# Optimization experiments

Hardware: AMD Instinct MI355X
Metric: run time of the kernel (lower is better)

Reference implementation:

```python
import jax, jax.numpy as jnp
import numpy as np

B, C, H, W = 8, 320, 32, 32
HEADS, DHEAD = 8, 40
CTX_LEN, CTX_DIM = 77, 768
FF_INNER = 4 * C
GROUPS = 32
HW = H * W


def setup_inputs() -> dict:
    key = jax.random.key(0)
    ks = jax.random.split(key, 16)
    def nrm(k, shape, s=0.02):
        return (jax.random.normal(k, shape) * s).astype(jnp.float32)
    z = lambda *s: jnp.zeros(s, jnp.float32)
    o = lambda *s: jnp.ones(s, jnp.float32)
    inp = {}
    inp["x"] = jax.random.normal(ks[0], (B, C, H, W), jnp.float32)
    inp["context"] = jax.random.normal(ks[1], (B, CTX_LEN, CTX_DIM), jnp.float32)
    inp["vis_mask"] = jax.random.uniform(ks[2], (B, HW, HW)) > 0.5
    inp["v2t_mask"] = jax.random.uniform(ks[3], (B, HW, CTX_LEN)) > 0.5
    inp["gn_scale"] = o(C); inp["gn_bias"] = z(C)
    inp["proj_in_w"] = nrm(ks[4], (C, C)); inp["proj_in_b"] = z(C)
    inp["n1_s"] = o(C); inp["n1_b"] = z(C)
    inp["wq1"] = nrm(ks[5], (C, C)); inp["wk1"] = nrm(ks[6], (C, C)); inp["wv1"] = nrm(ks[7], (C, C))
    inp["wo1"] = nrm(ks[8], (C, C)); inp["bo1"] = z(C)
    inp["n2_s"] = o(C); inp["n2_b"] = z(C)
    inp["wq2"] = nrm(ks[9], (C, C)); inp["wk2"] = nrm(ks[10], (CTX_DIM, C)); inp["wv2"] = nrm(ks[11], (CTX_DIM, C))
    inp["wo2"] = nrm(ks[12], (C, C)); inp["bo2"] = z(C)
    inp["n3_s"] = o(C); inp["n3_b"] = z(C)
    inp["ff_w1"] = nrm(ks[13], (C, 2 * FF_INNER)); inp["ff_b1"] = z(2 * FF_INNER)
    inp["ff_w2"] = nrm(ks[14], (FF_INNER, C)); inp["ff_b2"] = z(C)
    inp["proj_out_w"] = nrm(ks[15], (C, C)); inp["proj_out_b"] = z(C)
    return inp


def group_norm(x, scale, bias, eps=1e-6):
    b, c, h, w = x.shape
    xg = x.reshape(b, GROUPS, -1)
    mu = xg.mean(-1, keepdims=True)
    var = xg.var(-1, keepdims=True)
    xn = ((xg - mu) * jax.lax.rsqrt(var + eps)).reshape(b, c, h, w)
    return xn * scale[None, :, None, None] + bias[None, :, None, None]


def layer_norm(x, s, b, eps=1e-5):
    mu = x.mean(-1, keepdims=True)
    var = x.var(-1, keepdims=True)
    return (x - mu) * jax.lax.rsqrt(var + eps) * s + b


def mha(xq, ctx, wq, wk, wv, wo, bo, mask):
    # CrossAttention: manual einsum softmax with boolean mask broadcast over heads
    b, n, _ = xq.shape
    m = ctx.shape[1]
    split = lambda t: t.reshape(b, -1, HEADS, DHEAD).transpose(0, 2, 1, 3)
    q = split(xq @ wq)   # [b,h,n,d]
    k = split(ctx @ wk)  # [b,h,m,d]
    v = split(ctx @ wv)
    sim = jnp.einsum('bhid,bhjd->bhij', q, k) * (DHEAD ** -0.5)
    if mask is not None:
        sim = jnp.where(mask[:, None, :, :], sim, jnp.finfo(sim.dtype).min)
    attn = jax.nn.softmax(sim, axis=-1)
    out = jnp.einsum('bhij,bhjd->bhid', attn, v)
    out = out.transpose(0, 2, 1, 3).reshape(b, n, HEADS * DHEAD)
    return out @ wo + bo


def reference(x, context, vis_mask, v2t_mask, gn_scale, gn_bias, proj_in_w, proj_in_b,
              n1_s, n1_b, wq1, wk1, wv1, wo1, bo1,
              n2_s, n2_b, wq2, wk2, wv2, wo2, bo2,
              n3_s, n3_b, ff_w1, ff_b1, ff_w2, ff_b2,
              proj_out_w, proj_out_b):
    x_in = x
    h = group_norm(x, gn_scale, gn_bias)
    # 1x1 conv proj_in == per-pixel linear; flatten b c h w -> b (hw) c
    h = h.reshape(B, C, HW).transpose(0, 2, 1) @ proj_in_w + proj_in_b
    # masked self-attention (vis mask)
    h = h + mha(layer_norm(h, n1_s, n1_b), layer_norm(h, n1_s, n1_b),
                wq1, wk1, wv1, wo1, bo1, vis_mask)
    # masked cross-attention to text (v2t mask)
    h = h + mha(layer_norm(h, n2_s, n2_b), context,
                wq2, wk2, wv2, wo2, bo2, v2t_mask)
    # GEGLU feedforward (glu=True, mult=4)
    y = layer_norm(h, n3_s, n3_b) @ ff_w1 + ff_b1
    a, g = jnp.split(y, 2, axis=-1)
    h = h + (a * jax.nn.gelu(g, approximate=False)) @ ff_w2 + ff_b2
    # proj_out + residual
    out = (h @ proj_out_w + proj_out_b).transpose(0, 2, 1).reshape(B, C, H, W)
    return out + x_in
```

## Files before the change

### kernel.cpp

```cpp
#include <hip/hip_runtime.h>
#include <hip/hip_bf16.h>
#include <math.h>


#define Bsz   8
#define Cch   320
#define HW    1024
#define NTOK  (Bsz*HW)
#define HEADS 8
#define DHEAD 40
#define CTXL  77
#define CTXD  768
#define FFI   1280
#define MCTX  (Bsz*CTXL)
#define MCTXP 640

typedef unsigned short u16;
typedef unsigned long long u64;
typedef __attribute__((ext_vector_type(8))) u16    u16x8;
typedef __attribute__((ext_vector_type(8))) __bf16 bf16x8;
typedef __attribute__((ext_vector_type(4))) float  f32x4;

__device__ inline u16 f2b(float f) {
    unsigned u = __float_as_uint(f);
    return (u16)((u + 0x7FFFu + ((u >> 16) & 1u)) >> 16);
}

__global__ __launch_bounds__(256) void gn_apply(
    const float* __restrict__ x, const float* __restrict__ gnA,
    const float* __restrict__ gnB, u16* __restrict__ out)
{
    __shared__ u16 T[64*72];
    const int tid = threadIdx.x;
    const int c0 = blockIdx.x * 64;
    const int p0 = blockIdx.y * 64;
    const int b  = blockIdx.z;
    for (int e = tid; e < 512; e += 256) {
        int r = e >> 3, ch = e & 7;
        const float* src = x + ((size_t)(b*Cch + c0 + r))*HW + p0 + ch*8;
        float a  = gnA[b*Cch + c0 + r];
        float bb = gnB[b*Cch + c0 + r];
        float4 v0 = *(const float4*)src;
        float4 v1 = *(const float4*)(src + 4);
        u16x8 val;
        val[0] = f2b(v0.x*a + bb); val[1] = f2b(v0.y*a + bb);
        val[2] = f2b(v0.z*a + bb); val[3] = f2b(v0.w*a + bb);
        val[4] = f2b(v1.x*a + bb); val[5] = f2b(v1.y*a + bb);
        val[6] = f2b(v1.z*a + bb); val[7] = f2b(v1.w*a + bb);
        *(u16x8*)&T[r*72 + (ch ^ (r & 7))*8] = val;
    }
    __syncthreads();
    for (int e = tid; e < 4096; e += 256) {
        int p = e >> 6, c = e & 63;
        u16 v = T[c*72 + (((p >> 3) ^ (c & 7))*8) + (p & 7)];
        out[((size_t)(b*HW + p0 + p))*Cch + c0 + c] = v;
    }
}

__global__ __launch_bounds__(256) void layernorm_kernel(
    const float* __restrict__ in, const float* __restrict__ s,
    const float* __restrict__ bgain, u16* __restrict__ out)
{
    int t = blockIdx.x*4 + (threadIdx.x >> 6);
    int lane = threadIdx.x & 63;
    const float* row = in + (size_t)t*Cch;
    float v[5];
    float sum = 0.f, sq = 0.f;
    #pragma unroll
    for (int i = 0; i < 5; ++i) {
        v[i] = row[lane + 64*i];
        sum += v[i]; sq += v[i]*v[i];
    }
    #pragma unroll
    for (int off = 32; off > 0; off >>= 1) {
        sum += __shfl_xor(sum, off);
        sq  += __shfl_xor(sq,  off);
    }
    float mean = sum * (1.f/320.f);
    float var  = sq  * (1.f/320.f) - mean*mean;
    float inv  = rsqrtf(var + 1e-5f);
    u16* orow = out + (size_t)t*Cch;
    #pragma unroll
    for (int i = 0; i < 5; ++i) {
        int c = lane + 64*i;
        orow[c] = f2b((v[i]-mean)*inv*s[c] + bgain[c]);
    }
}

struct WDesc { const float* src; u16* dst; int K; int N; int tiles; float scl; };
struct WPack { WDesc w[12]; };

#define WT_TILES 620
#define CTXBLK   240

__global__ __launch_bounds__(256) void preamble(
    WPack p, const float* __restrict__ ctxsrc, u16* __restrict__ ctxdst,
    const void* __restrict__ vis, const void* __restrict__ v2t,
    u64* __restrict__ bvis, u64* __restrict__ bv2t,
    const float* __restrict__ x, const float* __restrict__ gscale,
    const float* __restrict__ gbias, float* __restrict__ gnA,
    float* __restrict__ gnB)
{
    __shared__ u16 T[64*72];
    int blk = blockIdx.x;
    int tid = threadIdx.x;
    if (blk < WT_TILES) {
        int t = blk;
        #pragma unroll
        for (int i = 0; i < 12; ++i) {
            int nt = p.w[i].tiles;
            if (t < nt) {
                const int K = p.w[i].K, N = p.w[i].N;
                const int ntN = N >> 6;
                const int tk = t / ntN, tn = t - tk*ntN;
                const float scl = p.w[i].scl;
                const float* src = p.w[i].src;
                u16* dst = p.w[i].dst;
                for (int e = tid; e < 512; e += 256) {
                    int r = e >> 3, ch = e & 7;
                    const float* sp = src + (size_t)(tk*64 + r)*N + tn*64 + ch*8;
                    float4 v0 = *(const float4*)sp;
                    float4 v1 = *(const float4*)(sp + 4);
                    u16x8 val;
                    val[0] = f2b(v0.x*scl); val[1] = f2b(v0.y*scl);
                    val[2] = f2b(v0.z*scl); val[3] = f2b(v0.w*scl);
                    val[4] = f2b(v1.x*scl); val[5] = f2b(v1.y*scl);
                    val[6] = f2b(v1.z*scl); val[7] = f2b(v1.w*scl);
                    *(u16x8*)&T[r*72 + (ch ^ (r & 7))*8] = val;
                }
                __syncthreads();
                for (int e = tid; e < 4096; e += 256) {
                    int n = e >> 6, k = e & 63;
                    u16 v = T[k*72 + (((n >> 3) ^ (k & 7))*8) + (n & 7)];
                    dst[(size_t)(tn*64 + n)*K + tk*64 + k] = v;
                }
                return;
            }
            t -= nt;
        }
        return;
    }
    if (blk < WT_TILES + CTXBLK) {
        int idx = (blk - WT_TILES)*2048 + tid*8;
        int r = idx / CTXD;
        u16x8 val = {};
        if (r < MCTX) {
            float4 v0 = *(const float4*)(ctxsrc + idx);
            float4 v1 = *(const float4*)(ctxsrc + idx + 4);
            val[0] = f2b(v0.x); val[1] = f2b(v0.y);
            val[2] = f2b(v0.z); val[3] = f2b(v0.w);
            val[4] = f2b(v1.x); val[5] = f2b(v1.y);
            val[6] = f2b(v1.z); val[7] = f2b(v1.w);
        }
        *(u16x8*)(ctxdst + idx) = val;
        return;
    }
    if (blk >= WT_TILES + CTXBLK + 4096) {
        int gb = blk - (WT_TILES + CTXBLK + 4096);
        int b = gb >> 5, g = gb & 31;
        __shared__ float rs[256], rq[256];
        const float4* xg = (const float4*)(x + ((size_t)b*Cch + g*10)*HW);
        float s = 0.f, q = 0.f;
        #pragma unroll
        for (int i = 0; i < 10; ++i) {
            float4 v = xg[tid + i*256];
            s += v.x + v.y + v.z + v.w;
            q += v.x*v.x + v.y*v.y + v.z*v.z + v.w*v.w;
        }
        rs[tid] = s; rq[tid] = q; __syncthreads();
        for (int off = 128; off > 0; off >>= 1) {
            if (tid < off) { rs[tid] += rs[tid+off]; rq[tid] += rq[tid+off]; }
            __syncthreads();
        }
        if (tid < 10) {
            float mean = rs[0] * (1.f/10240.f);
            float var  = rq[0] * (1.f/10240.f) - mean*mean;
            float inv  = rsqrtf(var + 1e-6f);
            int chn = g*10 + tid;
            float a = inv * gscale[chn];
            gnA[b*Cch + chn] = a;
            gnB[b*Cch + chn] = gbias[chn] - mean*a;
        }
        return;
    }
    __shared__ int any;
    if (tid == 0) any = 0;
    __syncthreads();
    const unsigned char* probe = (const unsigned char*)vis;
    for (int i = tid; i < 4096; i += 256)
        if ((i & 3) && probe[i]) any = 1;
    __syncthreads();
    const int isU8 = any;
    int mb = blk - WT_TILES - CTXBLK;
    const void* mask; u64* bits; int Lkv, nw;
    if (mb < 2048) { mask = vis; bits = bvis; Lkv = HW;   nw = 16; }
    else           { mask = v2t; bits = bv2t; Lkv = CTXL; nw = 2; mb -= 2048; }
    const int wv = tid >> 6, lane = tid & 63;
    const int row = mb*4 + wv;
    const unsigned char* m8  = (const unsigned char*)mask;
    const int*           m32 = (const int*)mask;
    const size_t base = (size_t)row * Lkv;
    for (int w = 0; w < nw; ++w) {
        int j = w*64 + lane;
        bool on = (j < Lkv) && (isU8 ? (m8[base+j] != 0) : (m32[base+j] != 0));
        u64 word = __ballot(on);
        if (lane == 0) bits[(size_t)row*nw + w] = word;
    }
}

__global__ __launch_bounds__(512) void gemm_bf16(
    const u16* __restrict__ A, const u16* __restrict__ Wt,
    const float* __restrict__ bias, const float* __restrict__ res,
    float* __restrict__ out, u16* __restrict__ out_bf, int M, int N, int K)
{
    __shared__ u16 As[2][128*40];
    __shared__ u16 Bs[2][64*40];
    const int tid  = threadIdx.x;
    const int lane = tid & 63;
    const int w    = tid >> 6;
    const int mp   = w >> 1;
    const int np   = w & 1;
    const int m0   = blockIdx.x * 128;
    const int n0   = blockIdx.y * 64;
    const int fr   = lane & 15, fg = lane >> 4;
    const int ar   = tid >> 2, ac = tid & 3;
    const bool hasB = tid < 256;

    const u16* pa = A  + (size_t)(m0 + ar)*K + ac*8;
    const u16* pb = Wt + (size_t)(n0 + ar)*K + ac*8;
    const int nk = K >> 5;

    *(u16x8*)&As[0][ar*40 + ac*8] = *(const u16x8*)pa;
    if (hasB) *(u16x8*)&Bs[0][ar*40 + ac*8] = *(const u16x8*)pb;
    u16x8 xa = *(const u16x8*)(pa + 32);
    u16x8 ya = *(const u16x8*)(pa + 64);
    u16x8 xb = {}, yb = {};
    if (hasB) { xb = *(const u16x8*)(pb + 32); yb = *(const u16x8*)(pb + 64); }

    f32x4 acc[2][2] = {};
    for (int i = 0; i < nk; i += 2) {
        __syncthreads();
        *(u16x8*)&As[1][ar*40 + ac*8] = xa;
        if (hasB) *(u16x8*)&Bs[1][ar*40 + ac*8] = xb;
        if (i + 3 < nk) {
            xa = *(const u16x8*)(pa + 32*(i+3));
            if (hasB) xb = *(const u16x8*)(pb + 32*(i+3));
        }
        {
            bf16x8 a0 = *(const bf16x8*)&As[0][(mp*32      + fr)*40 + fg*8];
            bf16x8 a1 = *(const bf16x8*)&As[0][(mp*32 + 16 + fr)*40 + fg*8];
            #pragma unroll
            for (int t = 0; t < 2; ++t) {
                bf16x8 b = *(const bf16x8*)&Bs[0][((np*2+t)*16 + fr)*40 + fg*8];
                acc[0][t] = __builtin_amdgcn_mfma_f32_16x16x32_bf16(a0, b, acc[0][t], 0, 0, 0);
                acc[1][t] = __builtin_amdgcn_mfma_f32_16x16x32_bf16(a1, b, acc[1][t], 0, 0, 0);
            }
        }
        __syncthreads();
        if (i + 2 < nk) {
            *(u16x8*)&As[0][ar*40 + ac*8] = ya;
            if (hasB) *(u16x8*)&Bs[0][ar*40 + ac*8] = yb;
            if (i + 4 < nk) {
                ya = *(const u16x8*)(pa + 32*(i+4));
                if (hasB) yb = *(const u16x8*)(pb + 32*(i+4));
            }
        }
        {
            bf16x8 a0 = *(const bf16x8*)&As[1][(mp*32      + fr)*40 + fg*8];
            bf16x8 a1 = *(const bf16x8*)&As[1][(mp*32 + 16 + fr)*40 + fg*8];
            #pragma unroll
            for (int t = 0; t < 2; ++t) {
                bf16x8 b = *(const bf16x8*)&Bs[1][((np*2+t)*16 + fr)*40 + fg*8];
                acc[0][t] = __builtin_amdgcn_mfma_f32_16x16x32_bf16(a0, b, acc[0][t], 0, 0, 0);
                acc[1][t] = __builtin_amdgcn_mfma_f32_16x16x32_bf16(a1, b, acc[1][t], 0, 0, 0);
            }
        }
    }
    #pragma unroll
    for (int at = 0; at < 2; ++at) {
        #pragma unroll
        for (int t = 0; t < 2; ++t) {
            int gn = n0 + (np*2+t)*16 + fr;
            float bv = bias ? bias[gn] : 0.f;
            #pragma unroll
            for (int i = 0; i < 4; ++i) {
                int gm = m0 + mp*32 + at*16 + fg*4 + i;
                float v = acc[at][t][i] + bv;
                if (res) v += res[(size_t)gm*N + gn];
                if (out) out[(size_t)gm*N + gn] = v;
                if (out_bf) out_bf[(size_t)gm*N + gn] = f2b(v);
            }
        }
    }
}

__global__ __launch_bounds__(512) void gemm_qkv_ctx(
    const u16* __restrict__ A, const u16* __restrict__ Wt,
    u16* __restrict__ out_bf,
    const u16* __restrict__ ctx, const u16* __restrict__ wk,
    const u16* __restrict__ wv, u16* __restrict__ kout, u16* __restrict__ vout)
{
    __shared__ u16 As[2][128*40];
    __shared__ u16 Bs[2][64*40];
    const int tid  = threadIdx.x;
    const int lane = tid & 63;
    const int w    = tid >> 6;
    const int fr   = lane & 15, fg = lane >> 4;
    const int bi   = blockIdx.x;

    if (bi < 960) {
        const int K  = Cch, N = 960;
        const int m0 = (bi & 63)*128;
        const int n0 = (bi >> 6)*64;
        const int mp = w >> 1, np = w & 1;
        const int ar = tid >> 2, ac = tid & 3;
        const bool hasB = tid < 256;

        const u16* pa = A  + (size_t)(m0 + ar)*K + ac*8;
        const u16* pb = Wt + (size_t)(n0 + ar)*K + ac*8;
        const int nk = K >> 5;

        *(u16x8*)&As[0][ar*40 + ac*8] = *(const u16x8*)pa;
        if (hasB) *(u16x8*)&Bs[0][ar*40 + ac*8] = *(const u16x8*)pb;
        u16x8 xa = *(const u16x8*)(pa + 32);
        u16x8 ya = *(const u16x8*)(pa + 64);
        u16x8 xb = {}, yb = {};
        if (hasB) { xb = *(const u16x8*)(pb + 32); yb = *(const u16x8*)(pb + 64); }

        f32x4 acc[2][2] = {};
        for (int i = 0; i < nk; i += 2) {
            __syncthreads();
            *(u16x8*)&As[1][ar*40 + ac*8] = xa;
            if (hasB) *(u16x8*)&Bs[1][ar*40 + ac*8] = xb;
            if (i + 3 < nk) {
                xa = *(const u16x8*)(pa + 32*(i+3));
                if (hasB) xb = *(const u16x8*)(pb + 32*(i+3));
            }
            {
                bf16x8 a0 = *(const bf16x8*)&As[0][(mp*32      + fr)*40 + fg*8];
                bf16x8 a1 = *(const bf16x8*)&As[0][(mp*32 + 16 + fr)*40 + fg*8];
                #pragma unroll
                for (int t = 0; t < 2; ++t) {
                    bf16x8 b = *(const bf16x8*)&Bs[0][((np*2+t)*16 + fr)*40 + fg*8];
                    acc[0][t] = __builtin_amdgcn_mfma_f32_16x16x32_bf16(a0, b, acc[0][t], 0, 0, 0);
                    acc[1][t] = __builtin_amdgcn_mfma_f32_16x16x32_bf16(a1, b, acc[1][t], 0, 0, 0);
                }
            }
            __syncthreads();
            if (i + 2 < nk) {
                *(u16x8*)&As[0][ar*40 + ac*8] = ya;
                if (hasB) *(u16x8*)&Bs[0][ar*40 + ac*8] = yb;
                if (i + 4 < nk) {
                    ya = *(const u16x8*)(pa + 32*(i+4));
                    if (hasB) yb = *(const u16x8*)(pb + 32*(i+4));
                }
            }
            {
                bf16x8 a0 = *(const bf16x8*)&As[1][(mp*32      + fr)*40 + fg*8];
                bf16x8 a1 = *(const bf16x8*)&As[1][(mp*32 + 16 + fr)*40 + fg*8];
                #pragma unroll
                for (int t = 0; t < 2; ++t) {
                    bf16x8 b = *(const bf16x8*)&Bs[1][((np*2+t)*16 + fr)*40 + fg*8];
                    acc[0][t] = __builtin_amdgcn_mfma_f32_16x16x32_bf16(a0, b, acc[0][t], 0, 0, 0);
                    acc[1][t] = __builtin_amdgcn_mfma_f32_16x16x32_bf16(a1, b, acc[1][t], 0, 0, 0);
                }
            }
        }
        #pragma unroll
        for (int at = 0; at < 2; ++at) {
            #pragma unroll
            for (int t = 0; t < 2; ++t) {
                int gn = n0 + (np*2+t)*16 + fr;
                #pragma unroll
                for (int i = 0; i < 4; ++i) {
                    int gm = m0 + mp*32 + at*16 + fg*4 + i;
                    out_bf[(size_t)gm*N + gn] = f2b(acc[at][t][i]);
                }
            }
        }
        return;
    }

    {
        int cb = bi - 960;
        const int z  = cb / 50; cb -= z*50;
        const int my = cb / 5, nx0 = cb - my*5;
        const int m0 = my*64, n0 = nx0*64;
        const u16* Wt2 = z ? wv : wk;
        u16* outp      = z ? vout : kout;
        const int mg = w >> 1;
        const int np = w & 1;
        const bool isA = tid < 256;
        const int cr = (tid & 255) >> 2, cc = tid & 3;

        const u16* ps = isA ? ctx + (size_t)(m0 + cr)*CTXD + cc*8
                            : Wt2 + (size_t)(n0 + cr)*CTXD + cc*8;
        u16* s0 = isA ? &As[0][cr*40 + cc*8] : &Bs[0][cr*40 + cc*8];
        u16* s1 = isA ? &As[1][cr*40 + cc*8] : &Bs[1][cr*40 + cc*8];
        const int nk = CTXD >> 5;

        *(u16x8*)s0 = *(const u16x8*)ps;
        u16x8 xv = *(const u16x8*)(ps + 32);
        u16x8 yv = *(const u16x8*)(ps + 64);

        f32x4 acc[2] = {};
        for (int i = 0; i < nk; i += 2) {
            __syncthreads();
            *(u16x8*)s1 = xv;
            if (i + 3 < nk) xv = *(const u16x8*)(ps + 32*(i+3));
            {
                bf16x8 a = *(const bf16x8*)&As[0][(mg*16 + fr)*40 + fg*8];
                #pragma unroll
                for (int t = 0; t < 2; ++t) {
                    bf16x8 b = *(const bf16x8*)&Bs[0][((np*2+t)*16 + fr)*40 + fg*8];
                    acc[t] = __builtin_amdgcn_mfma_f32_16x16x32_bf16(a, b, acc[t], 0, 0, 0);
                }
            }
            __syncthreads();
            if (i + 2 < nk) {
                *(u16x8*)s0 = yv;
                if (i + 4 < nk) yv = *(const u16x8*)(ps + 32*(i+4));
            }
            {
                bf16x8 a = *(const bf16x8*)&As[1][(mg*16 + fr)*40 + fg*8];
                #pragma unroll
                for (int t = 0; t < 2; ++t) {
                    bf16x8 b = *(const bf16x8*)&Bs[1][((np*2+t)*16 + fr)*40 + fg*8];
                    acc[t] = __builtin_amdgcn_mfma_f32_16x16x32_bf16(a, b, acc[t], 0, 0, 0);
                }
            }
        }
        #pragma unroll
        for (int t = 0; t < 2; ++t) {
            int gn = n0 + (np*2+t)*16 + fr;
            #pragma unroll
            for (int i = 0; i < 4; ++i) {
                int gm = m0 + mg*16 + fg*4 + i;
                if (gm < MCTX)
                    outp[(size_t)gm*Cch + gn] = f2b(acc[t][i]);
            }
        }
    }
}

__global__ __launch_bounds__(512) void gemm_pout(
    const u16* __restrict__ A, const u16* __restrict__ Wt,
    const float* __restrict__ bias, const float* __restrict__ x,
    float* __restrict__ out, int K)
{
    __shared__ u16 As[2][128*40];
    __shared__ u16 Bs[2][64*40];
    const int tid  = threadIdx.x;
    const int lane = tid & 63;
    const int w    = tid >> 6;
    const int mp   = w >> 1;
    const int np   = w & 1;
    const int m0   = blockIdx.x * 128;
    const int n0   = blockIdx.y * 64;
    const int fr   = lane & 15, fg = lane >> 4;
    const int ar   = tid >> 2, ac = tid & 3;
    const bool hasB = tid < 256;

    const u16* pa = A  + (size_t)(m0 + ar)*K + ac*8;
    const u16* pb = Wt + (size_t)(n0 + ar)*K + ac*8;
    const int nk = K >> 5;

    *(u16x8*)&As[0][ar*40 + ac*8] = *(const u16x8*)pa;
    if (hasB) *(u16x8*)&Bs[0][ar*40 + ac*8] = *(const u16x8*)pb;
    u16x8 xa = *(const u16x8*)(pa + 32);
    u16x8 ya = *(const u16x8*)(pa + 64);
    u16x8 xb = {}, yb = {};
    if (hasB) { xb = *(const u16x8*)(pb + 32); yb = *(const u16x8*)(pb + 64); }

    f32x4 acc[2][2] = {};
    for (int i = 0; i < nk; i += 2) {
        __syncthreads();
        *(u16x8*)&As[1][ar*40 + ac*8] = xa;
        if (hasB) *(u16x8*)&Bs[1][ar*40 + ac*8] = xb;
        if (i + 3 < nk) {
            xa = *(const u16x8*)(pa + 32*(i+3));
            if (hasB) xb = *(const u16x8*)(pb + 32*(i+3));
        }
        {
            bf16x8 a0 = *(const bf16x8*)&As[0][(mp*32      + fr)*40 + fg*8];
            bf16x8 a1 = *(const bf16x8*)&As[0][(mp*32 + 16 + fr)*40 + fg*8];
            #pragma unroll
            for (int t = 0; t < 2; ++t) {
                bf16x8 b = *(const bf16x8*)&Bs[0][((np*2+t)*16 + fr)*40 + fg*8];
                acc[0][t] = __builtin_amdgcn_mfma_f32_16x16x32_bf16(a0, b, acc[0][t], 0, 0, 0);
                acc[1][t] = __builtin_amdgcn_mfma_f32_16x16x32_bf16(a1, b, acc[1][t], 0, 0, 0);
            }
        }
        __syncthreads();
        if (i + 2 < nk) {
            *(u16x8*)&As[0][ar*40 + ac*8] = ya;
            if (hasB) *(u16x8*)&Bs[0][ar*40 + ac*8] = yb;
            if (i + 4 < nk) {
                ya = *(const u16x8*)(pa + 32*(i+4));
                if (hasB) yb = *(const u16x8*)(pb + 32*(i+4));
            }
        }
        {
            bf16x8 a0 = *(const bf16x8*)&As[1][(mp*32      + fr)*40 + fg*8];
            bf16x8 a1 = *(const bf16x8*)&As[1][(mp*32 + 16 + fr)*40 + fg*8];
            #pragma unroll
            for (int t = 0; t < 2; ++t) {
                bf16x8 b = *(const bf16x8*)&Bs[1][((np*2+t)*16 + fr)*40 + fg*8];
                acc[0][t] = __builtin_amdgcn_mfma_f32_16x16x32_bf16(a0, b, acc[0][t], 0, 0, 0);
                acc[1][t] = __builtin_amdgcn_mfma_f32_16x16x32_bf16(a1, b, acc[1][t], 0, 0, 0);
            }
        }
    }
    #pragma unroll
    for (int at = 0; at < 2; ++at) {
        #pragma unroll
        for (int t = 0; t < 2; ++t) {
            int gn = n0 + (np*2+t)*16 + fr;
            float bv = bias[gn];
            int gm0 = m0 + mp*32 + at*16 + fg*4;
            int b   = gm0 >> 10;
            int pcol= gm0 & (HW-1);
            size_t o = ((size_t)(b*Cch + gn))*HW + pcol;
            f32x4 xv = *(const f32x4*)&x[o];
            f32x4 vv;
            #pragma unroll
            for (int i = 0; i < 4; ++i) vv[i] = acc[at][t][i] + bv + xv[i];
            *(f32x4*)&out[o] = vv;
        }
    }
}

__global__ __launch_bounds__(512) void geglu_bf16(
    const u16* __restrict__ A, const u16* __restrict__ Wt,
    const float* __restrict__ b1, u16* __restrict__ out, int M, int K)
{
    __shared__ u16 As[2][128*40];
    __shared__ u16 Ba[2][64*40];
    __shared__ u16 Bg[2][64*40];
    const int tid  = threadIdx.x;
    const int lane = tid & 63;
    const int w    = tid >> 6;
    const int mp   = w >> 1;
    const int np   = w & 1;
    const int m0   = blockIdx.x * 128;
    const int n0   = blockIdx.y * 64;
    const int fr   = lane & 15, fg = lane >> 4;
    const int ar   = tid >> 2, ac = tid & 3;
    const int nk   = K >> 5;

    const u16* pa = A + (size_t)(m0 + ar)*K + ac*8;
    const int bq = (ar < 64) ? (n0 + ar) : (FFI + n0 + ar - 64);
    const u16* pb = Wt + (size_t)bq*K + ac*8;
    u16* bs0 = (ar < 64) ? &Ba[0][ar*40 + ac*8] : &Bg[0][(ar-64)*40 + ac*8];
    u16* bs1 = (ar < 64) ? &Ba[1][ar*40 + ac*8] : &Bg[1][(ar-64)*40 + ac*8];

    *(u16x8*)&As[0][ar*40 + ac*8] = *(const u16x8*)pa;
    *(u16x8*)bs0 = *(const u16x8*)pb;
    u16x8 xa = *(const u16x8*)(pa + 32);
    u16x8 xb = *(const u16x8*)(pb + 32);
    u16x8 ya = *(const u16x8*)(pa + 64);
    u16x8 yb = *(const u16x8*)(pb + 64);

    f32x4 aca[2][2] = {}, acg[2][2] = {};
    for (int i = 0; i < nk; i += 2) {
        __syncthreads();
        *(u16x8*)&As[1][ar*40 + ac*8] = xa;
        *(u16x8*)bs1 = xb;
        if (i + 3 < nk) {
            xa = *(const u16x8*)(pa + 32*(i+3));
            xb = *(const u16x8*)(pb + 32*(i+3));
        }
        {
            bf16x8 a0 = *(const bf16x8*)&As[0][(mp*32      + fr)*40 + fg*8];
            bf16x8 a1 = *(const bf16x8*)&As[0][(mp*32 + 16 + fr)*40 + fg*8];
            #pragma unroll
            for (int t = 0; t < 2; ++t) {
                bf16x8 ba = *(const bf16x8*)&Ba[0][((np*2+t)*16 + fr)*40 + fg*8];
                bf16x8 bg = *(const bf16x8*)&Bg[0][((np*2+t)*16 + fr)*40 + fg*8];
                aca[0][t] = __builtin_amdgcn_mfma_f32_16x16x32_bf16(a0, ba, aca[0][t], 0, 0, 0);
                aca[1][t] = __builtin_amdgcn_mfma_f32_16x16x32_bf16(a1, ba, aca[1][t], 0, 0, 0);
                acg[0][t] = __builtin_amdgcn_mfma_f32_16x16x32_bf16(a0, bg, acg[0][t], 0, 0, 0);
                acg[1][t] = __builtin_amdgcn_mfma_f32_16x16x32_bf16(a1, bg, acg[1][t], 0, 0, 0);
            }
        }
        __syncthreads();
        if (i + 2 < nk) {
            *(u16x8*)&As[0][ar*40 + ac*8] = ya;
            *(u16x8*)bs0 = yb;
            if (i + 4 < nk) {
                ya = *(const u16x8*)(pa + 32*(i+4));
                yb = *(const u16x8*)(pb + 32*(i+4));
            }
        }
        {
            bf16x8 a0 = *(const bf16x8*)&As[1][(mp*32      + fr)*40 + fg*8];
            bf16x8 a1 = *(const bf16x8*)&As[1][(mp*32 + 16 + fr)*40 + fg*8];
            #pragma unroll
            for (int t = 0; t < 2; ++t) {
                bf16x8 ba = *(const bf16x8*)&Ba[1][((np*2+t)*16 + fr)*40 + fg*8];
                bf16x8 bg = *(const bf16x8*)&Bg[1][((np*2+t)*16 + fr)*40 + fg*8];
                aca[0][t] = __builtin_amdgcn_mfma_f32_16x16x32_bf16(a0, ba, aca[0][t], 0, 0, 0);
                aca[1][t] = __builtin_amdgcn_mfma_f32_16x16x32_bf16(a1, ba, aca[1][t], 0, 0, 0);
                acg[0][t] = __builtin_amdgcn_mfma_f32_16x16x32_bf16(a0, bg, acg[0][t], 0, 0, 0);
                acg[1][t] = __builtin_amdgcn_mfma_f32_16x16x32_bf16(a1, bg, acg[1][t], 0, 0, 0);
            }
        }
    }
    #pragma unroll
    for (int at = 0; at < 2; ++at) {
        #pragma unroll
        for (int t = 0; t < 2; ++t) {
            int gn = n0 + (np*2+t)*16 + fr;
            float ba = b1[gn], bg = b1[FFI + gn];
            #pragma unroll
            for (int i = 0; i < 4; ++i) {
                int gm = m0 + mp*32 + at*16 + fg*4 + i;
                float av = aca[at][t][i] + ba;
                float gv = acg[at][t][i] + bg;
                float gel = 0.5f*gv*(1.f + erff(gv*0.70710678118654752f));
                out[(size_t)gm*FFI + gn] = f2b(av*gel);
            }
        }
    }
}

__global__ __launch_bounds__(256) void transpose_both(
    const u16* __restrict__ vself, u16* __restrict__ vt_self,
    const u16* __restrict__ vcross, u16* __restrict__ vt_cross)
{
    __shared__ u16 T[64*72];
    const int tid = threadIdx.x;
    const int bi  = blockIdx.x;
    const u16* in; u16* out; int istride, Ltok, ostride, c0, t0, b;
    if (bi < 640) {
        c0 = (bi % 5)*64; t0 = ((bi/5) & 15)*64; b = bi/80;
        in = vself;  istride = 960; Ltok = HW;   out = vt_self;  ostride = HW;
    } else {
        int cb = bi - 640;
        c0 = (cb % 5)*64; t0 = ((cb/5) & 1)*64;  b = cb/10;
        in = vcross; istride = Cch; Ltok = CTXL; out = vt_cross; ostride = 128;
    }
    for (int e = tid; e < 512; e += 256) {
        int r = e >> 3, ch = e & 7;
        u16x8 val = {};
        if (t0 + r < Ltok)
            val = *(const u16x8*)(in + ((size_t)(b*Ltok + t0 + r))*istride + c0 + ch*8);
        *(u16x8*)&T[r*72 + (ch ^ (r & 7))*8] = val;
    }
    __syncthreads();
    for (int e = tid; e < 4096; e += 256) {
        int c = e >> 6, t = e & 63;
        u16 v = T[t*72 + (((c >> 3) ^ (t & 7))*8) + (c & 7)];
        out[((size_t)(b*Cch + c0 + c))*ostride + t0 + t] = v;
    }
}

__global__ __launch_bounds__(512) void flash_mfma(
    const u16* __restrict__ qb, int qstride,
    const u16* __restrict__ kb, int kstride,
    const u16* __restrict__ vt, int vstride,
    const u64* __restrict__ mbits, int nw,
    u16* __restrict__ out,
    int Lkv)
{
    __shared__ u16 QPs[128*72];
    __shared__ u16 Ks[2][64*72];
    __shared__ u16 Vs[2][48*72];

    const int tid  = threadIdx.x;
    const int lane = tid & 63;
    const int w    = tid >> 6;
    const int col  = lane & 15;
    const int quad = lane >> 4;
    const int bi   = blockIdx.x;
    const int hb   = (bi & 7)*8 + (bi >> 6);
    const int qt   = (bi >> 3) & 7;
    const int h    = hb & 7;
    const int b    = hb >> 3;
    const int q0   = qt*128;
    const int ch   = tid & 7;
    const int r0   = tid >> 3;

    {
        const u16* qT = qb + ((size_t)(b*HW + q0))*qstride + (size_t)h*DHEAD + ch*8;
        u16x8 v0 = {}, v1 = {};
        if (ch < 5) {
            v0 = *(const u16x8*)(qT + (size_t)r0*qstride);
            v1 = *(const u16x8*)(qT + (size_t)(r0+64)*qstride);
        }
        *(u16x8*)&QPs[r0*72 + ch*8]      = v0;
        *(u16x8*)&QPs[(r0+64)*72 + ch*8] = v1;
    }
    if (tid < 128) {
        int rr  = tid >> 3;
        int row = 40 + (rr & 7);
        int buf = rr >> 3;
        u16x8 v = {};
        if (row == DHEAD) {
            #pragma unroll
            for (int z = 0; z < 8; ++z) v[z] = 0x3F80;
        }
        *(u16x8*)&Vs[buf][row*72 + ch*8] = v;
    }

    const bool kok = ch < 5;
    const u16* kR = kb + (size_t)b*Lkv*kstride + (size_t)h*DHEAD + ch*8
                       + (size_t)r0*kstride;
    const u16* vR = vt + ((size_t)(b*Cch + h*DHEAD))*vstride + ch*8
                       + (size_t)r0*vstride;
    const bool vok = r0 < DHEAD;
    const u64* mrow = mbits + ((size_t)(b*HW + q0 + w*16 + quad*4))*nw;

    u16x8 nk = {}, nv = {};
    if (kok && r0 < Lkv) nk = *(const u16x8*)kR;
    if (vok) nv = *(const u16x8*)vR;

    __syncthreads();
    const bf16x8 qa0 = *(const bf16x8*)&QPs[(w*16 + col)*72 +  0 + quad*8];
    const bf16x8 qa1 = *(const bf16x8*)&QPs[(w*16 + col)*72 + 32 + quad*8];

    f32x4 acc_o[3] = {};

    const int nkt = (Lkv + 63) / 64;
    int cur = 0;
    for (int jt = 0; jt < nkt; ++jt) {
        *(u16x8*)&Ks[cur][r0*72 + ch*8] = nk;
        if (vok) *(u16x8*)&Vs[cur][r0*72 + ch*8] = nv;
        if (jt + 1 < nkt) {
            kR += (size_t)64*kstride;
            vR += 64;
            nk = (u16x8){};
            if (kok && ((jt+1)*64 + r0 < Lkv)) nk = *(const u16x8*)kR;
            if (vok) nv = *(const u16x8*)vR;
        }
        __syncthreads();

        u64 mw[4];
        #pragma unroll
        for (int i = 0; i < 4; ++i) mw[i] = mrow[i*nw + jt];

        f32x4 s[4] = {};
        #pragma unroll
        for (int nt = 0; nt < 4; ++nt) {
            bf16x8 b0 = *(const bf16x8*)&Ks[cur][(nt*16 + col)*72 +  0 + quad*8];
            bf16x8 b1 = *(const bf16x8*)&Ks[cur][(nt*16 + col)*72 + 32 + quad*8];
            s[nt] = __builtin_amdgcn_mfma_f32_16x16x32_bf16(qa0, b0, s[nt], 0, 0, 0);
            s[nt] = __builtin_amdgcn_mfma_f32_16x16x32_bf16(qa1, b1, s[nt], 0, 0, 0);
        }

        #pragma unroll
        for (int i = 0; i < 4; ++i) {
            #pragma unroll
            for (int nt = 0; nt < 4; ++nt) {
                float p = __builtin_amdgcn_exp2f(s[nt][i]);
                unsigned bits = (unsigned)(mw[i] >> (nt*16));
                s[nt][i] = ((bits >> col) & 1u) ? p : 0.f;
            }
        }

        #pragma unroll
        for (int nt = 0; nt < 4; ++nt)
            #pragma unroll
            for (int i = 0; i < 4; ++i)
                QPs[(w*16 + quad*4 + i)*68 + nt*16 + col] =
                    (u16)(__float_as_uint(s[nt][i]) >> 16);

        bf16x8 pa0, pa1;
        __builtin_memcpy(&pa0, &QPs[(w*16 + col)*68 +  0 + quad*8], 16);
        __builtin_memcpy(&pa1, &QPs[(w*16 + col)*68 + 32 + quad*8], 16);
        #pragma unroll
        for (int nt = 0; nt < 3; ++nt) {
            bf16x8 vb0 = *(const bf16x8*)&Vs[cur][(nt*16 + col)*72 +  0 + quad*8];
            bf16x8 vb1 = *(const bf16x8*)&Vs[cur][(nt*16 + col)*72 + 32 + quad*8];
            acc_o[nt] = __builtin_amdgcn_mfma_f32_16x16x32_bf16(pa0, vb0, acc_o[nt], 0, 0, 0);
            acc_o[nt] = __builtin_amdgcn_mfma_f32_16x16x32_bf16(pa1, vb1, acc_o[nt], 0, 0, 0);
        }
        cur ^= 1;
    }

    float inv_l[4];
    #pragma unroll
    for (int i = 0; i < 4; ++i)
        inv_l[i] = 1.f / __shfl(acc_o[2][i], (lane & 48) | 8);

    #pragma unroll
    for (int nt = 0; nt < 3; ++nt) {
        int d = nt*16 + col;
        if (d < DHEAD) {
            #pragma unroll
            for (int i = 0; i < 4; ++i) {
                int q = q0 + w*16 + quad*4 + i;
                out[((size_t)(b*HW + q))*Cch + h*DHEAD + d] = f2b(acc_o[nt][i] * inv_l[i]);
            }
        }
    }
}

extern "C" void kernel_launch(void* const* d_in, const int* in_sizes, int n_in,
                              void* d_out, int out_size, void* d_ws, size_t ws_size,
                              hipStream_t stream)
{
    const float* x        = (const float*)d_in[0];
    const float* context  = (const float*)d_in[1];
    const void*  vis_mask = d_in[2];
    const void*  v2t_mask = d_in[3];
    const float* gn_s     = (const float*)d_in[4];
    const float* gn_b     = (const float*)d_in[5];
    const float* proj_in_w= (const float*)d_in[6];
    const float* proj_in_b= (const float*)d_in[7];
    const float* n1_s     = (const float*)d_in[8];
    const float* n1_b     = (const float*)d_in[9];
    const float* wq1      = (const float*)d_in[10];
    const float* wk1      = (const float*)d_in[11];
    const float* wv1      = (const float*)d_in[12];
    const float* wo1      = (const float*)d_in[13];
    const float* bo1      = (const float*)d_in[14];
    const float* n2_s     = (const float*)d_in[15];
    const float* n2_b     = (const float*)d_in[16];
    const float* wq2      = (const float*)d_in[17];
    const float* wk2      = (const float*)d_in[18];
    const float* wv2      = (const float*)d_in[19];
    const float* wo2      = (const float*)d_in[20];
    const float* bo2      = (const float*)d_in[21];
    const float* n3_s     = (const float*)d_in[22];
    const float* n3_b     = (const float*)d_in[23];
    const float* ff_w1    = (const float*)d_in[24];
    const float* ff_b1    = (const float*)d_in[25];
    const float* ff_w2    = (const float*)d_in[26];
    const float* ff_b2    = (const float*)d_in[27];
    const float* pout_w   = (const float*)d_in[28];
    const float* pout_b   = (const float*)d_in[29];
    float* out = (float*)d_out;

    const size_t TOKC = (size_t)NTOK*Cch;
    float* ws   = (float*)d_ws;
    float* Hb   = ws;
    u16*   QKV  = (u16*)(Hb + TOKC);
    u16*   Vt_g = QKV + 3*TOKC;
    u16*   G_bf = QKV;
    u16*   T0b  = Vt_g + TOKC;
    u16*   T1b  = T0b + TOKC;
    u16*   Hb_bf= T1b + TOKC;
    u16*   Wbf  = Hb_bf + TOKC;
    u64*   mb_vis = (u64*)(Wbf + 2539520);
    u64*   mb_v2t = mb_vis + 131072;
    u16*   ctx_bf = (u16*)(mb_v2t + 16384);
    u16*   Kc_bf  = ctx_bf + MCTXP*CTXD;
    u16*   Vc_bf  = Kc_bf + 640*Cch;
    float* gnA    = (float*)(Vc_bf + 640*Cch);
    float* gnB    = gnA + Bsz*Cch;
    u16*   Vt_x   = (u16*)(gnB + Bsz*Cch);

    u16* w_q1  = Wbf;
    u16* w_k1  = Wbf +  102400;
    u16* w_v1  = Wbf +  204800;
    u16* w_pin = Wbf +  307200;
    u16* w_o1  = Wbf +  409600;
    u16* w_q2  = Wbf +  512000;
    u16* w_o2  = Wbf +  614400;
    u16* w_ff1 = Wbf +  716800;
    u16* w_ff2 = Wbf + 1536000;
    u16* w_po  = Wbf + 1945600;
    u16* w_k2  = Wbf + 2048000;
    u16* w_v2  = Wbf + 2293760;

    const float qscale = 0.15811388300841897f * 1.4426950408889634f;
    WPack pack;
    pack.w[0]  = { wq1,       w_q1,  Cch, Cch, 25,  qscale };
    pack.w[1]  = { wk1,       w_k1,  Cch, Cch, 25,  1.f };
    pack.w[2]  = { wv1,       w_v1,  Cch, Cch, 25,  1.f };
    pack.w[3]  = { proj_in_w, w_pin, Cch, Cch, 25,  1.f };
    pack.w[4]  = { wo1,       w_o1,  Cch, Cch, 25,  1.f };
    pack.w[5]  = { wq2,       w_q2,  Cch, Cch, 25,  qscale };
    pack.w[6]  = { wo2,       w_o2,  Cch, Cch, 25,  1.f };
    pack.w[7]  = { ff_w1,     w_ff1, Cch, 2*FFI, 200, 1.f };
    pack.w[8]  = { ff_w2,     w_ff2, FFI, Cch, 100, 1.f };
    pack.w[9]  = { pout_w,    w_po,  Cch, Cch, 25,  1.f };
    pack.w[10] = { wk2,       w_k2,  CTXD, Cch, 60, 1.f };
    pack.w[11] = { wv2,       w_v2,  CTXD, Cch, 60, 1.f };

    dim3 blk256(256);
    dim3 blk512(512);
    dim3 gTok(NTOK/128, Cch/64);
    dim3 gFF(NTOK/128, FFI/64);
    dim3 gGN(Cch/64, HW/64, Bsz);

    preamble<<<WT_TILES + CTXBLK + 4096 + 256, blk256, 0, stream>>>(
        pack, context, ctx_bf, vis_mask, v2t_mask, mb_vis, mb_v2t,
        x, gn_s, gn_b, gnA, gnB);

    gn_apply<<<gGN, blk256, 0, stream>>>(x, gnA, gnB, T0b);
    gemm_bf16<<<gTok, blk512, 0, stream>>>(T0b, w_pin, proj_in_b, nullptr, Hb, nullptr, NTOK, Cch, Cch);

    layernorm_kernel<<<NTOK/4, blk256, 0, stream>>>(Hb, n1_s, n1_b, T0b);
    gemm_qkv_ctx<<<1060, blk512, 0, stream>>>(T0b, w_q1, QKV,
                                              ctx_bf, w_k2, w_v2, Kc_bf, Vc_bf);
    transpose_both<<<720, blk256, 0, stream>>>(QKV + 640, Vt_g, Vc_bf, Vt_x);
    flash_mfma<<<512, blk512, 0, stream>>>(QKV, 960, QKV + 320, 960, Vt_g, HW,
                                           mb_vis, 16, T1b, HW);
    gemm_bf16<<<gTok, blk512, 0, stream>>>(T1b, w_o1, bo1, Hb, Hb, nullptr, NTOK, Cch, Cch);

    layernorm_kernel<<<NTOK/4, blk256, 0, stream>>>(Hb, n2_s, n2_b, T0b);
    gemm_bf16<<<gTok, blk512, 0, stream>>>(T0b, w_q2, nullptr, nullptr, nullptr, QKV, NTOK, Cch, Cch);
    flash_mfma<<<512, blk512, 0, stream>>>(QKV, Cch, Kc_bf, Cch, Vt_x, 128,
                                           mb_v2t, 2, T1b, CTXL);
    gemm_bf16<<<gTok, blk512, 0, stream>>>(T1b, w_o2, bo2, Hb, Hb, nullptr, NTOK, Cch, Cch);

    layernorm_kernel<<<NTOK/4, blk256, 0, stream>>>(Hb, n3_s, n3_b, T0b);
    geglu_bf16<<<gFF, blk512, 0, stream>>>(T0b, w_ff1, ff_b1, G_bf, NTOK, Cch);
    gemm_bf16<<<gTok, blk512, 0, stream>>>(G_bf, w_ff2, ff_b2, Hb, nullptr, Hb_bf, NTOK, Cch, FFI);

    gemm_pout<<<gTok, blk512, 0, stream>>>(Hb_bf, w_po, pout_b, x, out, Cch);
}
```

Before: 353.9 us.

## Fuse self-attn V transpose into QKV GEMM epilogue, cross V transpose into flash

```diff
diff --git a/kernel.cpp b/kernel.cpp
--- a/kernel.cpp
+++ b/kernel.cpp
@@ -18,6 +18,7 @@
 typedef unsigned short u16;
 typedef unsigned long long u64;
 typedef __attribute__((ext_vector_type(8))) u16    u16x8;
+typedef __attribute__((ext_vector_type(4))) u16    u16x4;
 typedef __attribute__((ext_vector_type(8))) __bf16 bf16x8;
 typedef __attribute__((ext_vector_type(4))) float  f32x4;
 
@@ -296,7 +297,7 @@
 
 __global__ __launch_bounds__(512) void gemm_qkv_ctx(
     const u16* __restrict__ A, const u16* __restrict__ Wt,
-    u16* __restrict__ out_bf,
+    u16* __restrict__ out_bf, u16* __restrict__ vt_self,
     const u16* __restrict__ ctx, const u16* __restrict__ wk,
     const u16* __restrict__ wv, u16* __restrict__ kout, u16* __restrict__ vout)
 {
@@ -366,15 +367,32 @@
                 }
             }
         }
-        #pragma unroll
-        for (int at = 0; at < 2; ++at) {
-            #pragma unroll
-            for (int t = 0; t < 2; ++t) {
-                int gn = n0 + (np*2+t)*16 + fr;
+        if (n0 < 640) {
+            #pragma unroll
+            for (int at = 0; at < 2; ++at) {
                 #pragma unroll
-                for (int i = 0; i < 4; ++i) {
-                    int gm = m0 + mp*32 + at*16 + fg*4 + i;
-                    out_bf[(size_t)gm*N + gn] = f2b(acc[at][t][i]);
+                for (int t = 0; t < 2; ++t) {
+                    int gn = n0 + (np*2+t)*16 + fr;
+                    #pragma unroll
+                    for (int i = 0; i < 4; ++i) {
+                        int gm = m0 + mp*32 + at*16 + fg*4 + i;
+                        out_bf[(size_t)gm*N + gn] = f2b(acc[at][t][i]);
+                    }
+                }
+            }
+        } else {
+            #pragma unroll
+            for (int at = 0; at < 2; ++at) {
+                #pragma unroll
+                for (int t = 0; t < 2; ++t) {
+                    int c  = n0 - 640 + (np*2+t)*16 + fr;
+                    int gm0 = m0 + mp*32 + at*16 + fg*4;
+                    int b  = gm0 >> 10;
+                    int p  = gm0 & (HW-1);
+                    u16x4 vv;
+                    #pragma unroll
+                    for (int i = 0; i < 4; ++i) vv[i] = f2b(acc[at][t][i]);
+                    *(u16x4*)&vt_self[((size_t)(b*Cch + c))*HW + p] = vv;
                 }
             }
         }
@@ -624,55 +642,47 @@
     }
 }
 
-__global__ __launch_bounds__(256) void transpose_both(
-    const u16* __restrict__ vself, u16* __restrict__ vt_self,
-    const u16* __restrict__ vcross, u16* __restrict__ vt_cross)
-{
-    __shared__ u16 T[64*72];
-    const int tid = threadIdx.x;
-    const int bi  = blockIdx.x;
-    const u16* in; u16* out; int istride, Ltok, ostride, c0, t0, b;
-    if (bi < 640) {
-        c0 = (bi % 5)*64; t0 = ((bi/5) & 15)*64; b = bi/80;
-        in = vself;  istride = 960; Ltok = HW;   out = vt_self;  ostride = HW;
-    } else {
-        int cb = bi - 640;
-        c0 = (cb % 5)*64; t0 = ((cb/5) & 1)*64;  b = cb/10;
-        in = vcross; istride = Cch; Ltok = CTXL; out = vt_cross; ostride = 128;
-    }
-    for (int e = tid; e < 512; e += 256) {
-        int r = e >> 3, ch = e & 7;
-        u16x8 val = {};
-        if (t0 + r < Ltok)
-            val = *(const u16x8*)(in + ((size_t)(b*Ltok + t0 + r))*istride + c0 + ch*8);
-        *(u16x8*)&T[r*72 + (ch ^ (r & 7))*8] = val;
-    }
-    __syncthreads();
-    for (int e = tid; e < 4096; e += 256) {
-        int c = e >> 6, t = e & 63;
-        u16 v = T[t*72 + (((c >> 3) ^ (t & 7))*8) + (c & 7)];
-        out[((size_t)(b*Cch + c0 + c))*ostride + t0 + t] = v;
-    }
-}
-
 __global__ __launch_bounds__(512) void flash_mfma(
     const u16* __restrict__ qb, int qstride,
     const u16* __restrict__ kb, int kstride,
     const u16* __restrict__ vt, int vstride,
     const u64* __restrict__ mbits, int nw,
     u16* __restrict__ out,
-    int Lkv)
+    int Lkv,
+    const u16* __restrict__ tin, u16* __restrict__ tout)
 {
     __shared__ u16 QPs[128*72];
     __shared__ u16 Ks[2][64*72];
     __shared__ u16 Vs[2][48*72];
 
     const int tid  = threadIdx.x;
+    const int bi   = blockIdx.x;
+
+    if (bi >= 512) {
+        int cb = bi - 512;
+        const int c0 = (cb % 5)*64;
+        const int t0 = ((cb/5) & 1)*64;
+        const int b  = cb/10;
+        {
+            int r = tid >> 3, ch2 = tid & 7;
+            u16x8 val = {};
+            if (t0 + r < CTXL)
+                val = *(const u16x8*)(tin + ((size_t)(b*CTXL + t0 + r))*Cch + c0 + ch2*8);
+            *(u16x8*)&QPs[r*72 + (ch2 ^ (r & 7))*8] = val;
+        }
+        __syncthreads();
+        for (int e = tid; e < 4096; e += 512) {
+            int c = e >> 6, t = e & 63;
+            u16 v = QPs[t*72 + (((c >> 3) ^ (t & 7))*8) + (c & 7)];
+            tout[((size_t)(b*Cch + c0 + c))*128 + t0 + t] = v;
+        }
+        return;
+    }
+
     const int lane = tid & 63;
     const int w    = tid >> 6;
     const int col  = lane & 15;
     const int quad = lane >> 4;
-    const int bi   = blockIdx.x;
     const int hb   = (bi & 7)*8 + (bi >> 6);
     const int qt   = (bi >> 3) & 7;
     const int h    = hb & 7;
@@ -893,17 +903,16 @@
     gemm_bf16<<<gTok, blk512, 0, stream>>>(T0b, w_pin, proj_in_b, nullptr, Hb, nullptr, NTOK, Cch, Cch);
 
     layernorm_kernel<<<NTOK/4, blk256, 0, stream>>>(Hb, n1_s, n1_b, T0b);
-    gemm_qkv_ctx<<<1060, blk512, 0, stream>>>(T0b, w_q1, QKV,
+    gemm_qkv_ctx<<<1060, blk512, 0, stream>>>(T0b, w_q1, QKV, Vt_g,
                                               ctx_bf, w_k2, w_v2, Kc_bf, Vc_bf);
-    transpose_both<<<720, blk256, 0, stream>>>(QKV + 640, Vt_g, Vc_bf, Vt_x);
-    flash_mfma<<<512, blk512, 0, stream>>>(QKV, 960, QKV + 320, 960, Vt_g, HW,
-                                           mb_vis, 16, T1b, HW);
+    flash_mfma<<<512 + 80, blk512, 0, stream>>>(QKV, 960, QKV + 320, 960, Vt_g, HW,
+                                                mb_vis, 16, T1b, HW, Vc_bf, Vt_x);
     gemm_bf16<<<gTok, blk512, 0, stream>>>(T1b, w_o1, bo1, Hb, Hb, nullptr, NTOK, Cch, Cch);
 
     layernorm_kernel<<<NTOK/4, blk256, 0, stream>>>(Hb, n2_s, n2_b, T0b);
     gemm_bf16<<<gTok, blk512, 0, stream>>>(T0b, w_q2, nullptr, nullptr, nullptr, QKV, NTOK, Cch, Cch);
     flash_mfma<<<512, blk512, 0, stream>>>(QKV, Cch, Kc_bf, Cch, Vt_x, 128,
-                                           mb_v2t, 2, T1b, CTXL);
+                                           mb_v2t, 2, T1b, CTXL, nullptr, nullptr);
     gemm_bf16<<<gTok, blk512, 0, stream>>>(T1b, w_o2, bo2, Hb, Hb, nullptr, NTOK, Cch, Cch);
 
     layernorm_kernel<<<NTOK/4, blk256, 0, stream>>>(Hb, n3_s, n3_b, T0b);
```

Measured after the change: 349.1 us. About the same (-1.3%).
